# Kernel tuning notes

Measured on AMD Instinct MI355X. Metric: run time of the kernel, lower is better.

Reference implementation:

```python
import jax, jax.numpy as jnp
import numpy as np
import math

HIDDEN = 256
NUM_LAYERS = 3
NUM_TAU = 4
DT = 0.05
TAU_MIN, TAU_MAX = 0.01, 10.0
IN_SIZE = 128
OUT_SIZE = 64
B, S = 64, 2048


def setup_inputs() -> dict:
    key = jax.random.key(0)
    ks = jax.random.split(key, 16)
    H = HIDDEN
    def xavier(k, shape):
        fan_in, fan_out = shape[1], shape[0]
        lim = math.sqrt(6.0 / (fan_in + fan_out))
        return jax.random.uniform(k, shape, jnp.float32, -lim, lim)
    def ortho(k, n):
        a = jax.random.normal(k, (n, n), jnp.float32)
        q, r = jnp.linalg.qr(a)
        return q * jnp.sign(jnp.diag(r))[None, :]
    x = jax.random.normal(ks[0], (B, S, IN_SIZE), jnp.float32)
    # complexity_net: Linear(in,64) -> ReLU -> Linear(64,1) -> Sigmoid
    cw1 = xavier(ks[1], (64, IN_SIZE)); cb1 = jnp.zeros((64,), jnp.float32)
    cw2 = xavier(ks[2], (1, 64)); cb2 = jnp.zeros((1,), jnp.float32)
    # input projection
    pw = xavier(ks[3], (H, IN_SIZE)); pb = jnp.zeros((H,), jnp.float32)
    # per-layer recurrent params (stacked over layers)
    W_rec = jnp.stack([ortho(jax.random.fold_in(ks[4], i), H) for i in range(NUM_LAYERS)])
    W_in = jnp.stack([xavier(jax.random.fold_in(ks[5], i), (H, H)) for i in range(NUM_LAYERS)])
    bias = jnp.zeros((NUM_LAYERS, H), jnp.float32)
    tau_bands = jnp.tile(jnp.logspace(math.log10(TAU_MIN), math.log10(TAU_MAX), NUM_TAU, dtype=jnp.float32)[None, :], (NUM_LAYERS, 1))
    # tau_mixer: Linear(1, NUM_TAU) per layer -> weight [NUM_TAU,1] stored as [NUM_TAU]
    tmw = jax.random.uniform(ks[6], (NUM_LAYERS, NUM_TAU), jnp.float32, -1.0, 1.0)
    tmb = jax.random.uniform(ks[7], (NUM_LAYERS, NUM_TAU), jnp.float32, -1.0, 1.0)
    # output projection
    ow = xavier(ks[8], (OUT_SIZE, H)); ob = jnp.zeros((OUT_SIZE,), jnp.float32)
    return {"x": x, "cw1": cw1, "cb1": cb1, "cw2": cw2, "cb2": cb2,
            "pw": pw, "pb": pb, "W_rec": W_rec, "W_in": W_in, "bias": bias,
            "tau_bands": tau_bands, "tmw": tmw, "tmb": tmb, "ow": ow, "ob": ob}


def reference(x, cw1, cb1, cw2, cb2, pw, pb, W_rec, W_in, bias, tau_bands, tmw, tmb, ow, ob):
    # complexity net on time-mean of inputs -> [B, 1]
    comp = jax.nn.sigmoid(jax.nn.relu(x.mean(axis=1) @ cw1.T + cb1) @ cw2.T + cb2)
    h_seq = x @ pw.T + pb  # [B, S, H]
    hidden = jnp.zeros((x.shape[0], HIDDEN), x.dtype)
    for i in range(NUM_LAYERS):
        # tau_mixer: comp [B,1] * weight [NUM_TAU] -> logits [B, NUM_TAU]
        w = jax.nn.softmax(comp * tmw[i] + tmb[i], axis=-1)
        mixed_tau = jnp.sum(tau_bands[i] * w, axis=-1)          # [B]
        alpha = jnp.exp(-DT / mixed_tau)[:, None]               # [B,1] broadcast over H
        Wr, Wi, b = W_rec[i], W_in[i], bias[i]
        ext = h_seq @ Wi.T + b                                  # precompute input drive [B,S,H]
        def step(h, xt):
            act = jnp.tanh(h @ Wr.T + xt)
            h_new = alpha * h + (1.0 - alpha) * act
            return h_new, h_new
        hidden, outs = jax.lax.scan(step, hidden, ext.transpose(1, 0, 2))
        h_seq = outs.transpose(1, 0, 2)                         # [B,S,H]
    out = h_seq @ ow.T + ob                                     # [B,S,out]
    return out[:, -1]                                           # [B,out]
```

## Files before the change

### kernel.cpp

```cpp
#include <hip/hip_runtime.h>
#include <hip/hip_bf16.h>
#include <math.h>
#include <type_traits>

#define HIDDEN 256
#define SEQ 2048
#define BATCH 64
#define INSZ 128
#define OUTSZ 64
#define DTC 0.05f
#define CCH 32
#define CHS (SEQ / CCH)
#define TBLK (CHS / 32)

typedef _Float16 f16x8 __attribute__((ext_vector_type(8)));
typedef float f32x4 __attribute__((ext_vector_type(4)));

__global__ __launch_bounds__(1024) void prep_kernel(
    const float* __restrict__ x, const float* __restrict__ cw1, const float* __restrict__ cb1,
    const float* __restrict__ cw2, const float* __restrict__ cb2,
    const float* __restrict__ tau_b, const float* __restrict__ tmw, const float* __restrict__ tmb,
    float* __restrict__ alphas, float* __restrict__ h_carry)
{
    __shared__ float p_lds[8][128];
    __shared__ float xm[128];
    __shared__ float t1[64];
    int b = blockIdx.x;
    int tid = threadIdx.x;
    if (tid < 256) {
        h_carry[0 * 16384 + b * 256 + tid] = 0.f;
        h_carry[1 * 16384 + b * 256 + tid] = 0.f;
        h_carry[2 * 16384 + b * 256 + tid] = 0.f;
    }
    int c = tid & 127, sh = tid >> 7;
    const float* xb = x + (size_t)b * SEQ * INSZ;
    float s = 0.f;
    for (int t = sh * 256; t < (sh + 1) * 256; ++t) s += xb[(size_t)t * INSZ + c];
    p_lds[sh][c] = s;
    __syncthreads();
    if (tid < 128) {
        float m = 0.f;
        #pragma unroll
        for (int i = 0; i < 8; ++i) m += p_lds[i][tid];
        xm[tid] = m / (float)SEQ;
    }
    __syncthreads();
    if (tid < 64) {
        float acc = cb1[tid];
        for (int k = 0; k < 128; ++k) acc += xm[k] * cw1[tid * 128 + k];
        t1[tid] = fmaxf(acc, 0.f);
    }
    __syncthreads();
    if (tid == 0) {
        float acc = cb2[0];
        for (int k = 0; k < 64; ++k) acc += t1[k] * cw2[k];
        float comp = 1.f / (1.f + expf(-acc));
        for (int i = 0; i < 3; ++i) {
            float lg[4], mx = -1e30f;
            for (int j = 0; j < 4; ++j) { lg[j] = comp * tmw[i * 4 + j] + tmb[i * 4 + j]; mx = fmaxf(mx, lg[j]); }
            float den = 0.f;
            for (int j = 0; j < 4; ++j) { lg[j] = expf(lg[j] - mx); den += lg[j]; }
            float mt = 0.f;
            for (int j = 0; j < 4; ++j) mt += tau_b[i * 4 + j] * (lg[j] / den);
            alphas[i * 64 + b] = expf(-DTC / mt);
        }
    }
}

__global__ __launch_bounds__(128) void wf_kernel(
    const float* __restrict__ W_in0, const float* __restrict__ pw,
    const float* __restrict__ pb, const float* __restrict__ bias0,
    float* __restrict__ Wf, float* __restrict__ bf)
{
    __shared__ float wrow[256];
    int j = blockIdx.x, k = threadIdx.x;
    for (int m = k; m < 256; m += 128) wrow[m] = W_in0[j * 256 + m];
    __syncthreads();
    float s = 0.f;
    for (int m = 0; m < 256; ++m) s = fmaf(wrow[m], pw[m * 128 + k], s);
    Wf[j * 128 + k] = s;
    if (k == 0) {
        float sb = bias0[j];
        for (int m = 0; m < 256; ++m) sb = fmaf(wrow[m], pb[m], sb);
        bf[j] = sb;
    }
}

__device__ __forceinline__ unsigned pkrtz(float a, float b) {
    return __builtin_bit_cast(unsigned, __builtin_amdgcn_cvt_pkrtz(a, b));
}

__device__ __forceinline__ float fast_tanh(float x) {
    float ex = __expf(2.f * x);
    float r = __builtin_amdgcn_rcpf(ex + 1.f);
    return 1.f - 2.f * r;
}

__device__ __forceinline__ void barrier_lds_only() {
    asm volatile("s_waitcnt lgkmcnt(0)\n\ts_barrier" ::: "memory");
}

__global__ __launch_bounds__(256, 2) void gemm0_kernel(
    const float* __restrict__ Asrc,
    const float* __restrict__ W,
    const float* __restrict__ bias,
    float* __restrict__ C)
{
    constexpr int KD = 128, KT = 4, ROWB = 256;
    __shared__ alignas(16) char alds[32 * ROWB];
    const int tid = threadIdx.x;
    const int wave = tid >> 6, lane = tid & 63;
    const int bl = lane & 15, q = lane >> 4;
    const int m0 = blockIdx.x * 32;

    f16x8 bfrag[4][KT];
    float bv[4];
    #pragma unroll
    for (int nt = 0; nt < 4; ++nt) {
        int n = wave * 64 + nt * 16 + bl;
        const float* wr = W + (size_t)n * KD;
        #pragma unroll
        for (int kt = 0; kt < KT; ++kt) {
            const float4* wp = (const float4*)(wr + kt * 32 + q * 8);
            float4 u0 = wp[0], u1 = wp[1];
            uint4 u = { pkrtz(u0.x, u0.y), pkrtz(u0.z, u0.w),
                        pkrtz(u1.x, u1.y), pkrtz(u1.z, u1.w) };
            bfrag[nt][kt] = __builtin_bit_cast(f16x8, u);
        }
        bv[nt] = bias[n];
    }
    #pragma unroll
    for (int it = 0; it < 2; ++it) {
        int idx = tid + it * 256;
        int row = idx >> 4, chunk = idx & 15;
        const float4* sp = (const float4*)(Asrc + (size_t)(m0 + row) * KD + chunk * 8);
        float4 f0 = sp[0], f1 = sp[1];
        uint4 u = { pkrtz(f0.x, f0.y), pkrtz(f0.z, f0.w),
                    pkrtz(f1.x, f1.y), pkrtz(f1.z, f1.w) };
        *(uint4*)(alds + row * ROWB + ((chunk * 16) ^ ((row & 7) << 4))) = u;
    }
    __syncthreads();

    f32x4 acc[2][4];
    #pragma unroll
    for (int mt = 0; mt < 2; ++mt)
        #pragma unroll
        for (int nt = 0; nt < 4; ++nt) acc[mt][nt] = (f32x4){0.f, 0.f, 0.f, 0.f};
    #pragma unroll
    for (int kt = 0; kt < KT; ++kt) {
        int inner = kt * 64 + q * 16;
        f16x8 a0 = __builtin_bit_cast(f16x8,
            *(const uint4*)(alds + (0 * 16 + bl) * ROWB + (inner ^ ((bl & 7) << 4))));
        f16x8 a1 = __builtin_bit_cast(f16x8,
            *(const uint4*)(alds + (1 * 16 + bl) * ROWB + (inner ^ ((bl & 7) << 4))));
        #pragma unroll
        for (int nt = 0; nt < 4; ++nt) {
            acc[0][nt] = __builtin_amdgcn_mfma_f32_16x16x32_f16(a0, bfrag[nt][kt], acc[0][nt], 0, 0, 0);
            acc[1][nt] = __builtin_amdgcn_mfma_f32_16x16x32_f16(a1, bfrag[nt][kt], acc[1][nt], 0, 0, 0);
        }
    }
    #pragma unroll
    for (int mt = 0; mt < 2; ++mt)
        #pragma unroll
        for (int nt = 0; nt < 4; ++nt) {
            int col = wave * 64 + nt * 16 + bl;
            #pragma unroll
            for (int r = 0; r < 4; ++r)
                C[(size_t)(m0 + mt * 16 + q * 4 + r) * 256 + col] = acc[mt][nt][r] + bv[nt];
        }
}

__device__ __forceinline__ void scan_chunk(
    char* smem, float* buf, const float* __restrict__ W_rec,
    const float* __restrict__ alphas, float* __restrict__ h_carry,
    int b, int c, int write_all)
{
    _Float16 (*hlds)[256] = (_Float16 (*)[256])smem;
    const int tid = threadIdx.x;
    const int wave = tid >> 6, lane = tid & 63;
    const int bl = lane & 15, q = lane >> 4;
    const int mt_own = bl >> 2, r_own = bl & 3;
    const int m = wave * 64 + mt_own * 16 + q * 4 + r_own;

    f16x8 afrag[4][8];
    #pragma unroll
    for (int mt = 0; mt < 4; ++mt) {
        const float* wr = W_rec + (size_t)(wave * 64 + mt * 16 + bl) * 256;
        #pragma unroll
        for (int kt = 0; kt < 8; ++kt) {
            const float4* wp = (const float4*)(wr + kt * 32 + q * 8);
            float4 wa = wp[0], wb4 = wp[1];
            uint4 u = { pkrtz(wa.x, wa.y), pkrtz(wa.z, wa.w),
                        pkrtz(wb4.x, wb4.y), pkrtz(wb4.z, wb4.w) };
            afrag[mt][kt] = __builtin_bit_cast(f16x8, u);
        }
    }

    const float alpha = alphas[b], onema = 1.f - alpha;
    float* bb = buf + (size_t)b * SEQ * HIDDEN;
    const int t0 = c * CHS, tend = t0 + CHS;

    float h_reg = h_carry[b * 256 + m];
    hlds[0][m] = (_Float16)h_reg;
    float e_cur = bb[(size_t)t0 * HIDDEN + m];
    float e_n1  = bb[(size_t)(t0 + 1) * HIDDEN + m];
    __syncthreads();

    auto step = [&](auto CB, int t) {
        constexpr int CUR = decltype(CB)::value;
        const char* rb = (const char*)&hlds[CUR][0];
        uint4 bq0 = *(const uint4*)(rb + q * 16);
        uint4 bq1 = *(const uint4*)(rb + 64 + q * 16);
        uint4 bq2 = *(const uint4*)(rb + 128 + q * 16);
        uint4 bq3 = *(const uint4*)(rb + 192 + q * 16);
        uint4 bq4 = *(const uint4*)(rb + 256 + q * 16);
        uint4 bq5 = *(const uint4*)(rb + 320 + q * 16);
        uint4 bq6 = *(const uint4*)(rb + 384 + q * 16);
        uint4 bq7 = *(const uint4*)(rb + 448 + q * 16);
        float e_n2 = 0.f;
        if (t + 2 < tend) e_n2 = bb[(size_t)(t + 2) * HIDDEN + m];

        f32x4 a0 = {0.f,0.f,0.f,0.f}, a1 = {0.f,0.f,0.f,0.f};
        f32x4 a2 = {0.f,0.f,0.f,0.f}, a3 = {0.f,0.f,0.f,0.f};
        #define MSTEP(BQ, KT) { f16x8 bf = __builtin_bit_cast(f16x8, BQ);                  \
            a0 = __builtin_amdgcn_mfma_f32_16x16x32_f16(afrag[0][KT], bf, a0, 0, 0, 0);    \
            a1 = __builtin_amdgcn_mfma_f32_16x16x32_f16(afrag[1][KT], bf, a1, 0, 0, 0);    \
            a2 = __builtin_amdgcn_mfma_f32_16x16x32_f16(afrag[2][KT], bf, a2, 0, 0, 0);    \
            a3 = __builtin_amdgcn_mfma_f32_16x16x32_f16(afrag[3][KT], bf, a3, 0, 0, 0); }
        MSTEP(bq0, 0) MSTEP(bq1, 1) MSTEP(bq2, 2) MSTEP(bq3, 3)
        MSTEP(bq4, 4) MSTEP(bq5, 5) MSTEP(bq6, 6) MSTEP(bq7, 7)
        #undef MSTEP

        f32x4 am = (mt_own == 0) ? a0 : (mt_own == 1) ? a1 : (mt_own == 2) ? a2 : a3;
        float s  = (r_own == 0) ? am[0] : (r_own == 1) ? am[1] : (r_own == 2) ? am[2] : am[3];

        float act = fast_tanh(s + e_cur);
        h_reg = alpha * h_reg + onema * act;
        hlds[CUR ^ 1][m] = (_Float16)h_reg;
        if (write_all)
            *((_Float16*)(bb + (size_t)t * HIDDEN) + m) = (_Float16)h_reg;
        barrier_lds_only();
        e_cur = e_n1;
        e_n1 = e_n2;
    };

    for (int t = t0; t < tend; t += 2) {
        step(std::integral_constant<int, 0>{}, t);
        step(std::integral_constant<int, 1>{}, t + 1);
    }
    h_carry[b * 256 + m] = h_reg;
}

__device__ __forceinline__ void gemm_chunk(
    char* smem, float* buf, const float* __restrict__ W,
    const float* __restrict__ bias, int g, int c)
{
    constexpr int KD = 256, KT = 8, ROWB = 512;
    char* alds = smem;
    const int tid = threadIdx.x;
    const int wave = tid >> 6, lane = tid & 63;
    const int bl = lane & 15, q = lane >> 4;
    const size_t m0 = (size_t)(g / TBLK) * SEQ + c * CHS + (g % TBLK) * 32;

    f16x8 bfrag[4][KT];
    float bv[4];
    #pragma unroll
    for (int nt = 0; nt < 4; ++nt) {
        int n = wave * 64 + nt * 16 + bl;
        const float* wr = W + (size_t)n * KD;
        #pragma unroll
        for (int kt = 0; kt < KT; ++kt) {
            const float4* wp = (const float4*)(wr + kt * 32 + q * 8);
            float4 u0 = wp[0], u1 = wp[1];
            uint4 u = { pkrtz(u0.x, u0.y), pkrtz(u0.z, u0.w),
                        pkrtz(u1.x, u1.y), pkrtz(u1.z, u1.w) };
            bfrag[nt][kt] = __builtin_bit_cast(f16x8, u);
        }
        bv[nt] = bias[n];
    }
    #pragma unroll
    for (int it = 0; it < 8; ++it) {
        int idx = tid + it * 256;
        int row = idx >> 5, chunk = idx & 31;
        uint4 u = *(const uint4*)((const char*)buf + (m0 + row) * 1024 + chunk * 16);
        *(uint4*)(alds + row * ROWB + ((chunk * 16) ^ ((row & 7) << 4))) = u;
    }
    __syncthreads();

    f32x4 acc[2][4];
    #pragma unroll
    for (int mt = 0; mt < 2; ++mt)
        #pragma unroll
        for (int nt = 0; nt < 4; ++nt) acc[mt][nt] = (f32x4){0.f, 0.f, 0.f, 0.f};
    #pragma unroll
    for (int kt = 0; kt < KT; ++kt) {
        int inner = kt * 64 + q * 16;
        f16x8 a0 = __builtin_bit_cast(f16x8,
            *(const uint4*)(alds + (0 * 16 + bl) * ROWB + (inner ^ ((bl & 7) << 4))));
        f16x8 a1 = __builtin_bit_cast(f16x8,
            *(const uint4*)(alds + (1 * 16 + bl) * ROWB + (inner ^ ((bl & 7) << 4))));
        #pragma unroll
        for (int nt = 0; nt < 4; ++nt) {
            acc[0][nt] = __builtin_amdgcn_mfma_f32_16x16x32_f16(a0, bfrag[nt][kt], acc[0][nt], 0, 0, 0);
            acc[1][nt] = __builtin_amdgcn_mfma_f32_16x16x32_f16(a1, bfrag[nt][kt], acc[1][nt], 0, 0, 0);
        }
    }
    #pragma unroll
    for (int mt = 0; mt < 2; ++mt)
        #pragma unroll
        for (int nt = 0; nt < 4; ++nt) {
            int col = wave * 64 + nt * 16 + bl;
            #pragma unroll
            for (int r = 0; r < 4; ++r)
                buf[(m0 + mt * 16 + q * 4 + r) * 256 + col] = acc[mt][nt][r] + bv[nt];
        }
}

__global__ __launch_bounds__(256, 1) void stage_kernel(
    int stage, float* buf,
    const float* __restrict__ W_rec, const float* __restrict__ W_in,
    const float* __restrict__ bias,  const float* __restrict__ alphas,
    float* __restrict__ h_carry)
{
    __shared__ alignas(16) char smem[16384];
    int blk = blockIdx.x;
    if (blk < 192) {
        int layer = blk >> 6;
        int c = stage - 2 * layer;
        if (c < 0 || c >= CCH) return;
        scan_chunk(smem, buf, W_rec + (size_t)layer * 65536, alphas + layer * 64,
                   h_carry + (size_t)layer * 16384, blk & 63, c, layer < 2);
    } else {
        int g = blk - 192;
        int which = g / (64 * TBLK);
        int gl = g % (64 * TBLK);
        int c = stage - 1 - 2 * which;
        if (c < 0 || c >= CCH) return;
        int lw = which + 1;
        gemm_chunk(smem, buf, W_in + (size_t)lw * 65536, bias + lw * 256, gl, c);
    }
}

__global__ __launch_bounds__(256) void outproj_kernel(
    const float* __restrict__ h_carry, const float* __restrict__ ow, const float* __restrict__ ob,
    float* __restrict__ out)
{
    __shared__ float h_l[256];
    __shared__ float p_lds[4][64];
    int b = blockIdx.x;
    int tid = threadIdx.x;
    h_l[tid] = h_carry[b * 256 + tid];
    __syncthreads();
    int o = tid & 63, qq = tid >> 6;
    float s = 0.f;
    const float4* wp = (const float4*)(ow + o * 256 + qq * 64);
    const float4* hp = (const float4*)(h_l + qq * 64);
    #pragma unroll
    for (int m = 0; m < 16; ++m) {
        float4 wv = wp[m]; float4 hv = hp[m];
        s = fmaf(wv.x, hv.x, s); s = fmaf(wv.y, hv.y, s);
        s = fmaf(wv.z, hv.z, s); s = fmaf(wv.w, hv.w, s);
    }
    p_lds[qq][o] = s;
    __syncthreads();
    if (tid < 64)
        out[b * 64 + tid] = p_lds[0][tid] + p_lds[1][tid] + p_lds[2][tid] + p_lds[3][tid] + ob[tid];
}

extern "C" void kernel_launch(void* const* d_in, const int* in_sizes, int n_in,
                              void* d_out, int out_size, void* d_ws, size_t ws_size,
                              hipStream_t stream)
{
    const float* x     = (const float*)d_in[0];
    const float* cw1   = (const float*)d_in[1];
    const float* cb1   = (const float*)d_in[2];
    const float* cw2   = (const float*)d_in[3];
    const float* cb2   = (const float*)d_in[4];
    const float* pw    = (const float*)d_in[5];
    const float* pb    = (const float*)d_in[6];
    const float* W_rec = (const float*)d_in[7];
    const float* W_in  = (const float*)d_in[8];
    const float* bias  = (const float*)d_in[9];
    const float* tau_b = (const float*)d_in[10];
    const float* tmw   = (const float*)d_in[11];
    const float* tmb   = (const float*)d_in[12];
    const float* ow    = (const float*)d_in[13];
    const float* ob    = (const float*)d_in[14];
    float* out = (float*)d_out;

    char* ws = (char*)d_ws;
    float* alphas  = (float*)ws;
    float* h_carry = (float*)(ws + 4096);
    float* bf      = (float*)(ws + 262144);
    float* Wf      = (float*)(ws + 266240);
    float* buf     = (float*)(ws + 1048576);

    const int MROWS = BATCH * SEQ;
    const int NGBLK = 192 + 2 * 64 * TBLK;

    prep_kernel<<<64, 1024, 0, stream>>>(x, cw1, cb1, cw2, cb2, tau_b, tmw, tmb, alphas, h_carry);
    wf_kernel<<<256, 128, 0, stream>>>(W_in, pw, pb, bias, Wf, bf);

    gemm0_kernel<<<MROWS / 32, 256, 0, stream>>>(x, Wf, bf, buf);

    for (int s = 0; s < CCH + 4; ++s)
        stage_kernel<<<NGBLK, 256, 0, stream>>>(s, buf, W_rec, W_in, bias, alphas, h_carry);

    outproj_kernel<<<64, 256, 0, stream>>>(h_carry + 2 * 16384, ow, ob, out);
}
```

Measured before the change: 1.623 ms.

## Stage GEMM0 output through LDS, split scan MFMA chains, enlarge gemm_chunk tile

gemm0 now writes its accumulator tile into shared memory and stores it to global with coalesced 16-byte writes, replacing scattered scalar stores. The recurrent scan step splits its K reduction into two independent MFMA accumulator chains that are summed at the end, which shortens the dependent MFMA chain on the serial critical path. gemm_chunk now processes a full 64-row chunk per block instead of 32-row tiles, halving the number of GEMM blocks and reusing each loaded weight fragment across twice as many rows. In exchange, register pressure and shared memory use per block go up, and occupancy may fall.

Result: slower. 1.818 ms (+12.0%).

```diff
diff --git a/kernel.cpp b/kernel.cpp
--- a/kernel.cpp
+++ b/kernel.cpp
@@ -11,7 +11,6 @@
 #define DTC 0.05f
 #define CCH 32
 #define CHS (SEQ / CCH)
-#define TBLK (CHS / 32)
 
 typedef _Float16 f16x8 __attribute__((ext_vector_type(8)));
 typedef float f32x4 __attribute__((ext_vector_type(4)));
@@ -108,6 +107,7 @@
 {
     constexpr int KD = 128, KT = 4, ROWB = 256;
     __shared__ alignas(16) char alds[32 * ROWB];
+    __shared__ alignas(16) float ctile[32 * 256];
     const int tid = threadIdx.x;
     const int wave = tid >> 6, lane = tid & 63;
     const int bl = lane & 15, q = lane >> 4;
@@ -166,8 +166,15 @@
             int col = wave * 64 + nt * 16 + bl;
             #pragma unroll
             for (int r = 0; r < 4; ++r)
-                C[(size_t)(m0 + mt * 16 + q * 4 + r) * 256 + col] = acc[mt][nt][r] + bv[nt];
-        }
+                ctile[(mt * 16 + q * 4 + r) * 256 + col] = acc[mt][nt][r] + bv[nt];
+        }
+    __syncthreads();
+    #pragma unroll
+    for (int it = 0; it < 8; ++it) {
+        int idx = tid + it * 256;
+        int row = idx >> 6, seg = idx & 63;
+        *(uint4*)(C + (size_t)(m0 + row) * 256 + seg * 4) = *(const uint4*)(ctile + row * 256 + seg * 4);
+    }
 }
 
 __device__ __forceinline__ void scan_chunk(
@@ -220,21 +227,31 @@
         float e_n2 = 0.f;
         if (t + 2 < tend) e_n2 = bb[(size_t)(t + 2) * HIDDEN + m];
 
-        f32x4 a0 = {0.f,0.f,0.f,0.f}, a1 = {0.f,0.f,0.f,0.f};
-        f32x4 a2 = {0.f,0.f,0.f,0.f}, a3 = {0.f,0.f,0.f,0.f};
-        #define MSTEP(BQ, KT) { f16x8 bf = __builtin_bit_cast(f16x8, BQ);                  \
-            a0 = __builtin_amdgcn_mfma_f32_16x16x32_f16(afrag[0][KT], bf, a0, 0, 0, 0);    \
-            a1 = __builtin_amdgcn_mfma_f32_16x16x32_f16(afrag[1][KT], bf, a1, 0, 0, 0);    \
-            a2 = __builtin_amdgcn_mfma_f32_16x16x32_f16(afrag[2][KT], bf, a2, 0, 0, 0);    \
-            a3 = __builtin_amdgcn_mfma_f32_16x16x32_f16(afrag[3][KT], bf, a3, 0, 0, 0); }
-        MSTEP(bq0, 0) MSTEP(bq1, 1) MSTEP(bq2, 2) MSTEP(bq3, 3)
-        MSTEP(bq4, 4) MSTEP(bq5, 5) MSTEP(bq6, 6) MSTEP(bq7, 7)
-        #undef MSTEP
-
-        f32x4 am = (mt_own == 0) ? a0 : (mt_own == 1) ? a1 : (mt_own == 2) ? a2 : a3;
-        float s  = (r_own == 0) ? am[0] : (r_own == 1) ? am[1] : (r_own == 2) ? am[2] : am[3];
-
-        float act = fast_tanh(s + e_cur);
+        f32x4 ya0 = {0.f,0.f,0.f,0.f}, ya1 = {0.f,0.f,0.f,0.f};
+        f32x4 ya2 = {0.f,0.f,0.f,0.f}, ya3 = {0.f,0.f,0.f,0.f};
+        f32x4 yb0 = {0.f,0.f,0.f,0.f}, yb1 = {0.f,0.f,0.f,0.f};
+        f32x4 yb2 = {0.f,0.f,0.f,0.f}, yb3 = {0.f,0.f,0.f,0.f};
+        #define MSTEPA(BQ, KT) { f16x8 bf = __builtin_bit_cast(f16x8, BQ);                   \
+            ya0 = __builtin_amdgcn_mfma_f32_16x16x32_f16(afrag[0][KT], bf, ya0, 0, 0, 0);    \
+            ya1 = __builtin_amdgcn_mfma_f32_16x16x32_f16(afrag[1][KT], bf, ya1, 0, 0, 0);    \
+            ya2 = __builtin_amdgcn_mfma_f32_16x16x32_f16(afrag[2][KT], bf, ya2, 0, 0, 0);    \
+            ya3 = __builtin_amdgcn_mfma_f32_16x16x32_f16(afrag[3][KT], bf, ya3, 0, 0, 0); }
+        #define MSTEPB(BQ, KT) { f16x8 bf = __builtin_bit_cast(f16x8, BQ);                   \
+            yb0 = __builtin_amdgcn_mfma_f32_16x16x32_f16(afrag[0][KT], bf, yb0, 0, 0, 0);    \
+            yb1 = __builtin_amdgcn_mfma_f32_16x16x32_f16(afrag[1][KT], bf, yb1, 0, 0, 0);    \
+            yb2 = __builtin_amdgcn_mfma_f32_16x16x32_f16(afrag[2][KT], bf, yb2, 0, 0, 0);    \
+            yb3 = __builtin_amdgcn_mfma_f32_16x16x32_f16(afrag[3][KT], bf, yb3, 0, 0, 0); }
+        MSTEPA(bq0, 0) MSTEPB(bq4, 4) MSTEPA(bq1, 1) MSTEPB(bq5, 5)
+        MSTEPA(bq2, 2) MSTEPB(bq6, 6) MSTEPA(bq3, 3) MSTEPB(bq7, 7)
+        #undef MSTEPA
+        #undef MSTEPB
+
+        f32x4 am = (mt_own == 0) ? ya0 : (mt_own == 1) ? ya1 : (mt_own == 2) ? ya2 : ya3;
+        f32x4 bm = (mt_own == 0) ? yb0 : (mt_own == 1) ? yb1 : (mt_own == 2) ? yb2 : yb3;
+        float sa = (r_own == 0) ? am[0] : (r_own == 1) ? am[1] : (r_own == 2) ? am[2] : am[3];
+        float sb = (r_own == 0) ? bm[0] : (r_own == 1) ? bm[1] : (r_own == 2) ? bm[2] : bm[3];
+
+        float act = fast_tanh(sa + sb + e_cur);
         h_reg = alpha * h_reg + onema * act;
         hlds[CUR ^ 1][m] = (_Float16)h_reg;
         if (write_all)
@@ -260,7 +277,7 @@
     const int tid = threadIdx.x;
     const int wave = tid >> 6, lane = tid & 63;
     const int bl = lane & 15, q = lane >> 4;
-    const size_t m0 = (size_t)(g / TBLK) * SEQ + c * CHS + (g % TBLK) * 32;
+    const size_t m0 = (size_t)g * SEQ + (size_t)c * CHS;
 
     f16x8 bfrag[4][KT];
     float bv[4];
@@ -287,26 +304,25 @@
     }
     __syncthreads();
 
-    f32x4 acc[2][4];
-    #pragma unroll
-    for (int mt = 0; mt < 2; ++mt)
+    f32x4 acc[4][4];
+    #pragma unroll
+    for (int mt = 0; mt < 4; ++mt)
         #pragma unroll
         for (int nt = 0; nt < 4; ++nt) acc[mt][nt] = (f32x4){0.f, 0.f, 0.f, 0.f};
     #pragma unroll
     for (int kt = 0; kt < KT; ++kt) {
         int inner = kt * 64 + q * 16;
-        f16x8 a0 = __builtin_bit_cast(f16x8,
-            *(const uint4*)(alds + (0 * 16 + bl) * ROWB + (inner ^ ((bl & 7) << 4))));
-        f16x8 a1 = __builtin_bit_cast(f16x8,
-            *(const uint4*)(alds + (1 * 16 + bl) * ROWB + (inner ^ ((bl & 7) << 4))));
-        #pragma unroll
-        for (int nt = 0; nt < 4; ++nt) {
-            acc[0][nt] = __builtin_amdgcn_mfma_f32_16x16x32_f16(a0, bfrag[nt][kt], acc[0][nt], 0, 0, 0);
-            acc[1][nt] = __builtin_amdgcn_mfma_f32_16x16x32_f16(a1, bfrag[nt][kt], acc[1][nt], 0, 0, 0);
-        }
-    }
-    #pragma unroll
-    for (int mt = 0; mt < 2; ++mt)
+        #pragma unroll
+        for (int mt = 0; mt < 4; ++mt) {
+            f16x8 a = __builtin_bit_cast(f16x8,
+                *(const uint4*)(alds + (mt * 16 + bl) * ROWB + (inner ^ ((bl & 7) << 4))));
+            #pragma unroll
+            for (int nt = 0; nt < 4; ++nt)
+                acc[mt][nt] = __builtin_amdgcn_mfma_f32_16x16x32_f16(a, bfrag[nt][kt], acc[mt][nt], 0, 0, 0);
+        }
+    }
+    #pragma unroll
+    for (int mt = 0; mt < 4; ++mt)
         #pragma unroll
         for (int nt = 0; nt < 4; ++nt) {
             int col = wave * 64 + nt * 16 + bl;
@@ -322,7 +338,7 @@
     const float* __restrict__ bias,  const float* __restrict__ alphas,
     float* __restrict__ h_carry)
 {
-    __shared__ alignas(16) char smem[16384];
+    __shared__ alignas(16) char smem[32768];
     int blk = blockIdx.x;
     if (blk < 192) {
         int layer = blk >> 6;
@@ -332,8 +348,8 @@
                    h_carry + (size_t)layer * 16384, blk & 63, c, layer < 2);
     } else {
         int g = blk - 192;
-        int which = g / (64 * TBLK);
-        int gl = g % (64 * TBLK);
+        int which = g >> 6;
+        int gl = g & 63;
         int c = stage - 1 - 2 * which;
         if (c < 0 || c >= CCH) return;
         int lw = which + 1;
@@ -396,7 +412,7 @@
     float* buf     = (float*)(ws + 1048576);
 
     const int MROWS = BATCH * SEQ;
-    const int NGBLK = 192 + 2 * 64 * TBLK;
+    const int NGBLK = 192 + 128;
 
     prep_kernel<<<64, 1024, 0, stream>>>(x, cw1, cb1, cw2, cb2, tau_b, tmw, tmb, alphas, h_carry);
     wf_kernel<<<256, 128, 0, stream>>>(W_in, pw, pb, bias, Wf, bf);
```
